# Kernel optimization log

Hardware: AMD Instinct MI355X
Metric: run time of the kernel (lower is better)

The kernel has to match this reference:

```python
import jax, jax.numpy as jnp
import numpy as np

B, T, E, H, N = 256, 8, 768, 768, 20000


def setup_inputs() -> dict:
    key = jax.random.key(0)
    ks = jax.random.split(key, 10)
    s = lambda k, shape, sc=1.0: jax.random.normal(k, shape, dtype=jnp.float32) * sc
    return {
        "current_sample_encodings": s(ks[0], (B, E)),
        "example_encodings": s(ks[1], (B, T, E)),
        "all_example_encodings": s(ks[2], (N, E)),
        "policy_example_indices": jax.random.randint(ks[3], (B, T), 0, N, dtype=jnp.int32),
        "W_init": s(ks[4], (E, H), E ** -0.5),
        "b_init": jnp.zeros((H,), jnp.float32),
        "Wx": s(ks[5], (E, 3 * H), E ** -0.5),
        "Wh": s(ks[6], (H, 3 * H), H ** -0.5),
        "bx": jnp.zeros((3 * H,), jnp.float32),
        "bh": jnp.zeros((3 * H,), jnp.float32),
        "bilinear": s(ks[7], (H, E), H ** -0.5),
        "vfe_w": s(ks[8], (H,), H ** -0.5),
        "vfe_b": jnp.zeros((), jnp.float32),
    }


def reference(current_sample_encodings, example_encodings, all_example_encodings,
              policy_example_indices, W_init, b_init, Wx, Wh, bx, bh,
              bilinear, vfe_w, vfe_b):
    Bb, Tt, Ee = example_encodings.shape

    # --- get_latent_states: GRU over example encodings, h0 from current sample ---
    h0 = jnp.tanh(current_sample_encodings @ W_init + b_init)  # [B,H]

    def gru_step(h, x):
        gx = x @ Wx + bx                      # [B,3H]
        gh = h @ Wh + bh                      # [B,3H]
        xr, xz, xn = jnp.split(gx, 3, axis=-1)
        hr, hz, hn = jnp.split(gh, 3, axis=-1)
        r = jax.nn.sigmoid(xr + hr)
        z = jax.nn.sigmoid(xz + hz)
        n = jnp.tanh(xn + r * hn)
        h_new = (1.0 - z) * n + z * h
        return h_new, h_new

    xs = jnp.swapaxes(example_encodings[:, :-1], 0, 1)   # [T-1,B,E]
    _, hs = jax.lax.scan(gru_step, h0, xs)               # [T-1,B,H]
    latent = jnp.concatenate([h0[None], hs], axis=0)     # [T,B,H]

    # --- bilinear query vectors and scoring against the full corpus ---
    query = jnp.einsum('tbh,he->tbe', latent, bilinear)          # [T,B,E]
    acts = jnp.einsum('tbe,ne->tbn', query, all_example_encodings)  # [T,B,N]

    # --- fused scatter masking: -inf at indices of previously chosen examples ---
    neg_inf = jnp.float32(-jnp.inf)

    def mask_step(used, inp):
        a_t, idx_t = inp                                  # [B,N], [B]
        out = jnp.where(used, neg_inf, a_t)
        used = used.at[jnp.arange(Bb), idx_t].set(True)
        return used, out

    used0 = jnp.zeros((Bb, acts.shape[-1]), dtype=bool)
    idxs = jnp.swapaxes(policy_example_indices, 0, 1)     # [T,B]
    _, masked = jax.lax.scan(mask_step, used0, (acts, idxs))  # [T,B,N]

    activations = jnp.swapaxes(masked, 0, 1).reshape(Bb * Tt, -1)  # [B*T,N]

    latent_bt = jnp.swapaxes(latent, 0, 1)                # [B,T,H]
    value_estimates = (latent_bt @ vfe_w + vfe_b).reshape(-1)  # [B*T]
    return activations, value_estimates
```

## Files before the change

### kernel.cpp

```cpp
#include <hip/hip_runtime.h>
#include <math.h>
#include <float.h>

constexpr int Bb = 256, Tt = 8, Ee = 768, Hh = 768, Nn = 20000;
constexpr int H3 = 3 * Hh;

__device__ inline float mask_val() { return __uint_as_float(0xFF7F0000u); }

typedef __attribute__((ext_vector_type(8))) short bf16x8;
typedef __attribute__((ext_vector_type(4))) float f32x4;

__device__ inline unsigned short bf16rne(float x) {
    unsigned u = __float_as_uint(x);
    return (unsigned short)((u + 0x7FFFu + ((u >> 16) & 1)) >> 16);
}
__device__ inline unsigned pk2(float a, float b) {
    return (unsigned)bf16rne(a) | ((unsigned)bf16rne(b) << 16);
}
__device__ inline float sigm(float x) { return 1.f / (1.f + expf(-x)); }

__device__ inline void glds16(const void* g, void* l) {
    __builtin_amdgcn_global_load_lds(
        (const __attribute__((address_space(1))) void*)g,
        (__attribute__((address_space(3))) void*)l, 16, 0, 0);
}

__global__ __launch_bounds__(256) void cvt_all(const float* __restrict__ a, unsigned* __restrict__ oa, int na8,
                                               const float* __restrict__ b, unsigned* __restrict__ ob, int nb8,
                                               const float* __restrict__ c, unsigned* __restrict__ oc, int nc8)
{
    int i = blockIdx.x * 256 + threadIdx.x;
    const float* src; unsigned* dst;
    if (i < na8)            { src = a; dst = oa; }
    else if (i < na8 + nb8) { i -= na8; src = b; dst = ob; }
    else                    { i -= na8 + nb8; if (i >= nc8) return; src = c; dst = oc; }
    const float4* p = (const float4*)(src + (size_t)i * 8);
    float4 x = p[0], y = p[1];
    uint4 v;
    v.x = pk2(x.x, x.y); v.y = pk2(x.z, x.w);
    v.z = pk2(y.x, y.y); v.w = pk2(y.z, y.w);
    *(uint4*)(dst + (size_t)i * 4) = v;
}

__global__ __launch_bounds__(256) void trans4(const float* __restrict__ Wi,
                                              const float* __restrict__ Wx,
                                              const float* __restrict__ Wh,
                                              const float* __restrict__ bil,
                                              unsigned short* __restrict__ WiT,
                                              unsigned short* __restrict__ WxT,
                                              unsigned short* __restrict__ WhG,
                                              unsigned short* __restrict__ bilT)
{
    __shared__ float tile[32][33];
    int b = blockIdx.x;
    const float* in; unsigned short* outp; int C; bool wh = false; int bx, by;
    if (b < 576)       { in = Wi;  outp = WiT;  C = Ee; bx = b % 24; by = b / 24; }
    else if (b < 2304) { b -= 576;  in = Wx;  outp = WxT;  C = H3; bx = b % 72; by = b / 72; }
    else if (b < 4032) { b -= 2304; in = Wh;  outp = WhG;  C = H3; bx = b % 72; by = b / 72; wh = true; }
    else               { b -= 4032; in = bil; outp = bilT; C = Hh; bx = b % 24; by = b / 24; }

    int c0 = bx * 32, r0 = by * 32;
    int t = threadIdx.x;
    int row = t >> 3, c4 = (t & 7) * 4;
    float4 v = *(const float4*)(in + (size_t)(r0 + row) * C + c0 + c4);
    tile[row][c4+0] = v.x; tile[row][c4+1] = v.y;
    tile[row][c4+2] = v.z; tile[row][c4+3] = v.w;
    __syncthreads();
    int crow = t >> 3, r4 = (t & 7) * 4;
    int cc = c0 + crow;
    int orow;
    if (wh) {
        int g = cc / Hh, ch = cc - g * Hh;
        orow = (ch >> 6) * 192 + g * 64 + (ch & 63);
    } else {
        orow = cc;
    }
    ushort4 o;
    o.x = bf16rne(tile[r4+0][crow]);
    o.y = bf16rne(tile[r4+1][crow]);
    o.z = bf16rne(tile[r4+2][crow]);
    o.w = bf16rne(tile[r4+3][crow]);
    *(ushort4*)(outp + (size_t)orow * 768 + r0 + r4) = o;
}

__global__ __launch_bounds__(256) void gemm_big64(const unsigned short* __restrict__ A,
                                                  const unsigned short* __restrict__ B,
                                                  float* __restrict__ C)
{
    constexpr int BUF = 32768;
    __shared__ char lds[2 * BUF];
    const int t = threadIdx.x;
    const int l = t & 63, w = t >> 6;
    const int wm = (w >> 1) * 64, wn = (w & 1) * 64;

    int id = (blockIdx.x & 7) * 314 + (blockIdx.x >> 3);
    const int bm = (id & 15) * 128;
    const int bn = (id >> 4) * 128;

    const int srow = t >> 3, sslot = t & 7;
    const char* gA[4]; const char* gB[4];
    #pragma unroll
    for (int p = 0; p < 4; ++p) {
        int rp = p * 32 + srow;
        int oct = sslot ^ ((rp >> 1) & 7);
        gA[p] = (const char*)A + (size_t)(bm + rp) * (Ee * 2) + oct * 16;
        int gn = bn + rp; if (gn > Nn - 1) gn = Nn - 1;
        gB[p] = (const char*)B + (size_t)gn * (Ee * 2) + oct * 16;
    }
    const int dbase = t * 16;

    int rAo[4][2], rBo[4][2];
    #pragma unroll
    for (int i = 0; i < 4; ++i) {
        int Ra = wm + i * 16 + (l & 15);
        int Rb = wn + i * 16 + (l & 15);
        #pragma unroll
        for (int ko = 0; ko < 2; ++ko) {
            rAo[i][ko] = Ra * 128 + ((((l >> 4) + 4 * ko) ^ ((Ra >> 1) & 7)) * 16);
            rBo[i][ko] = 16384 + Rb * 128 + ((((l >> 4) + 4 * ko) ^ ((Rb >> 1) & 7)) * 16);
        }
    }

    f32x4 acc[4][4];
    #pragma unroll
    for (int i = 0; i < 4; ++i)
        #pragma unroll
        for (int j = 0; j < 4; ++j)
            acc[i][j] = (f32x4){0.f, 0.f, 0.f, 0.f};

    #pragma unroll
    for (int p = 0; p < 4; ++p) {
        glds16(gA[p], lds + p * 4096 + dbase);
        glds16(gB[p], lds + 16384 + p * 4096 + dbase);
    }
    __syncthreads();

    int cur = 0;
    for (int kt = 0; kt < 12; ++kt) {
        if (kt + 1 < 12) {
            int kb = (kt + 1) * 128;
            char* nb = lds + (cur ^ 1) * BUF;
            #pragma unroll
            for (int p = 0; p < 4; ++p) {
                glds16(gA[p] + kb, nb + p * 4096 + dbase);
                glds16(gB[p] + kb, nb + 16384 + p * 4096 + dbase);
            }
        }
        const char* base = lds + cur * BUF;
        bf16x8 af[4][2], bf[4][2];
        #pragma unroll
        for (int i = 0; i < 4; ++i)
            #pragma unroll
            for (int ko = 0; ko < 2; ++ko) {
                af[i][ko] = *(const bf16x8*)(base + rAo[i][ko]);
                bf[i][ko] = *(const bf16x8*)(base + rBo[i][ko]);
            }
        #pragma unroll
        for (int ko = 0; ko < 2; ++ko)
            #pragma unroll
            for (int i = 0; i < 4; ++i)
                #pragma unroll
                for (int j = 0; j < 4; ++j)
                    acc[i][j] = __builtin_amdgcn_mfma_f32_16x16x32_bf16(af[i][ko], bf[j][ko], acc[i][j], 0, 0, 0);
        __syncthreads();
        cur ^= 1;
    }

    #pragma unroll
    for (int i = 0; i < 4; ++i) {
        int gm = bm + wm + i * 16 + (l >> 4) * 4;
        #pragma unroll
        for (int j = 0; j < 4; ++j) {
            int gn = bn + wn + j * 16 + (l & 15);
            if (gn < Nn) {
                #pragma unroll
                for (int q = 0; q < 4; ++q)
                    C[(size_t)(gm + q) * Nn + gn] = acc[i][j][q];
            }
        }
    }
}

template<int TM, bool CLAMP, bool BIAS, int ACT, int OMODE>
__global__ __launch_bounds__(256) void gemm_mfma(const unsigned short* __restrict__ A, int lda,
                                                 const unsigned short* __restrict__ B,
                                                 const float* __restrict__ bias,
                                                 float* __restrict__ C, int ldc,
                                                 unsigned short* __restrict__ Cbf,
                                                 int M, int N, int K, int nsec)
{
    constexpr int AG  = (TM >= 64) ? TM / 64 : 1;
    constexpr int AB  = TM * 64;
    constexpr int BUF = (TM + 128) * 64;
    constexpr int FM  = (TM >= 64) ? 4 : 2;
    constexpr int FN  = (TM == 128) ? 4 : 2;
    __shared__ char lds[2 * BUF];
    const int t = threadIdx.x;

    int by, bx;
    {
        int id = ((blockIdx.x & 7) * (gridDim.x >> 3)) + (blockIdx.x >> 3);
        by = id / nsec; bx = id - by * nsec;
    }
    const int bm = by * TM, bn = bx * 128;

    const int l = t & 63, w = t >> 6;
    const int wm = (TM == 128) ? (w >> 1) * 64 : 0;
    const int wn = (TM == 128) ? (w & 1) * 64 : w * 32;

    const int sr = w * 16 + (l >> 2);
    const int slot = l & 3;

    const char* gA[AG]; int lA[AG];
    #pragma unroll
    for (int p = 0; p < AG; ++p) {
        int r = p * 64 + sr;
        int rr = (TM == 32) ? (r & 31) : r;
        int oct = slot ^ ((rr >> 1) & 3);
        gA[p] = (const char*)A + (size_t)(bm + rr) * lda * 2 + oct * 16;
        lA[p] = p * 4096 + w * 1024;
    }
    const char* gB[2]; int lB[2];
    #pragma unroll
    for (int p = 0; p < 2; ++p) {
        int r = p * 64 + sr;
        int oct = slot ^ ((r >> 1) & 3);
        int gn = bn + r;
        if (CLAMP) gn = (gn > N - 1) ? (N - 1) : gn;
        gB[p] = (const char*)B + (size_t)gn * K * 2 + oct * 16;
        lB[p] = AB + p * 4096 + w * 1024;
    }

    int rAo[FM], rBo[FN];
    #pragma unroll
    for (int i = 0; i < FM; ++i) {
        int Ra = wm + i * 16 + (l & 15);
        rAo[i] = Ra * 64 + (((l >> 4) ^ ((Ra >> 1) & 3)) * 16);
    }
    #pragma unroll
    for (int j = 0; j < FN; ++j) {
        int Rb = wn + j * 16 + (l & 15);
        rBo[j] = AB + Rb * 64 + (((l >> 4) ^ ((Rb >> 1) & 3)) * 16);
    }

    f32x4 acc[FM][FN];
    #pragma unroll
    for (int i = 0; i < FM; ++i)
        #pragma unroll
        for (int j = 0; j < FN; ++j)
            acc[i][j] = (f32x4){0.f, 0.f, 0.f, 0.f};

    if (TM > 32 || w < 2) {
        #pragma unroll
        for (int p = 0; p < AG; ++p) glds16(gA[p], lds + lA[p]);
    }
    #pragma unroll
    for (int p = 0; p < 2;  ++p) glds16(gB[p], lds + lB[p]);
    __syncthreads();

    int cur = 0;
    for (int k0 = 0; k0 < K; k0 += 32) {
        if (k0 + 32 < K) {
            int kb = (k0 + 32) * 2;
            char* nb = lds + (cur ^ 1) * BUF;
            if (TM > 32 || w < 2) {
                #pragma unroll
                for (int p = 0; p < AG; ++p) glds16(gA[p] + kb, nb + lA[p]);
            }
            #pragma unroll
            for (int p = 0; p < 2;  ++p) glds16(gB[p] + kb, nb + lB[p]);
        }
        const char* base = lds + cur * BUF;
        bf16x8 af[FM], bf[FN];
        #pragma unroll
        for (int i = 0; i < FM; ++i) af[i] = *(const bf16x8*)(base + rAo[i]);
        #pragma unroll
        for (int j = 0; j < FN; ++j) bf[j] = *(const bf16x8*)(base + rBo[j]);
        #pragma unroll
        for (int i = 0; i < FM; ++i)
            #pragma unroll
            for (int j = 0; j < FN; ++j)
                acc[i][j] = __builtin_amdgcn_mfma_f32_16x16x32_bf16(af[i], bf[j], acc[i][j], 0, 0, 0);
        __syncthreads();
        cur ^= 1;
    }

    #pragma unroll
    for (int i = 0; i < FM; ++i) {
        int gm = bm + wm + i * 16 + (l >> 4) * 4;
        #pragma unroll
        for (int j = 0; j < FN; ++j) {
            int gn = bn + wn + j * 16 + (l & 15);
            if (!CLAMP || gn < N) {
                #pragma unroll
                for (int q = 0; q < 4; ++q) {
                    float v = acc[i][j][q];
                    if (BIAS) v += bias[gn];
                    if (ACT == 1) v = tanhf(v);
                    if (OMODE & 1) C[(size_t)(gm + q) * ldc + gn] = v;
                    if (OMODE & 2) Cbf[(size_t)(gm + q) * ldc + gn] = bf16rne(v);
                }
            }
        }
    }
}

__global__ __launch_bounds__(256) void gru_fused(const unsigned short* __restrict__ latbf_t,
                                                 const unsigned short* __restrict__ WhG,
                                                 const float* __restrict__ gx_t,
                                                 const float* __restrict__ bh,
                                                 const float* __restrict__ latent_t,
                                                 float* __restrict__ latent_t1,
                                                 unsigned short* __restrict__ latbf_t1)
{
    constexpr int LDA = Tt * Hh;
    constexpr int LDG = Tt * H3;
    constexpr int ABY = 4096;
    constexpr int BUF = ABY + 24576;
    __shared__ char lds[2 * BUF];
    const int t = threadIdx.x;
    const int mb = blockIdx.x & 7, cb = blockIdx.x >> 3;
    const int bm = mb * 32;

    const int l = t & 63, w = t >> 6;
    const int srow = t >> 3;
    const int sslot = t & 7;

    const char* gA = (const char*)latbf_t + (size_t)(bm + srow) * (LDA * 2)
                   + ((sslot ^ ((srow >> 1) & 7)) * 16);
    const int dA = w * 1024;

    const char* gB[6]; int dB[6];
    #pragma unroll
    for (int p = 0; p < 6; ++p) {
        int rp = p * 32 + srow;
        gB[p] = (const char*)WhG + (size_t)(cb * 192 + rp) * (Hh * 2)
              + ((sslot ^ ((rp >> 1) & 7)) * 16);
        dB[p] = ABY + p * 4096 + w * 1024;
    }

    int rAo[2][2], rBo[3][2];
    #pragma unroll
    for (int i = 0; i < 2; ++i) {
        int Ra = i * 16 + (l & 15);
        #pragma unroll
        for (int ko = 0; ko < 2; ++ko)
            rAo[i][ko] = Ra * 128 + ((((l >> 4) + 4 * ko) ^ ((Ra >> 1) & 7)) * 16);
    }
    #pragma unroll
    for (int g = 0; g < 3; ++g) {
        int Rb = g * 64 + w * 16 + (l & 15);
        #pragma unroll
        for (int ko = 0; ko < 2; ++ko)
            rBo[g][ko] = ABY + Rb * 128 + ((((l >> 4) + 4 * ko) ^ ((Rb >> 1) & 7)) * 16);
    }

    f32x4 acc[2][3];
    #pragma unroll
    for (int i = 0; i < 2; ++i)
        #pragma unroll
        for (int g = 0; g < 3; ++g)
            acc[i][g] = (f32x4){0.f, 0.f, 0.f, 0.f};

    glds16(gA, lds + dA);
    #pragma unroll
    for (int p = 0; p < 6; ++p) glds16(gB[p], lds + dB[p]);
    __syncthreads();

    int cur = 0;
    for (int kt = 0; kt < 12; ++kt) {
        if (kt + 1 < 12) {
            int kb = (kt + 1) * 128;
            char* nb = lds + (cur ^ 1) * BUF;
            glds16(gA + kb, nb + dA);
            #pragma unroll
            for (int p = 0; p < 6; ++p) glds16(gB[p] + kb, nb + dB[p]);
        }
        const char* base = lds + cur * BUF;
        bf16x8 af[2][2], bfr[3][2];
        #pragma unroll
        for (int i = 0; i < 2; ++i)
            #pragma unroll
            for (int ko = 0; ko < 2; ++ko) af[i][ko] = *(const bf16x8*)(base + rAo[i][ko]);
        #pragma unroll
        for (int g = 0; g < 3; ++g)
            #pragma unroll
            for (int ko = 0; ko < 2; ++ko) bfr[g][ko] = *(const bf16x8*)(base + rBo[g][ko]);
        #pragma unroll
        for (int ko = 0; ko < 2; ++ko)
            #pragma unroll
            for (int i = 0; i < 2; ++i)
                #pragma unroll
                for (int g = 0; g < 3; ++g)
                    acc[i][g] = __builtin_amdgcn_mfma_f32_16x16x32_bf16(af[i][ko], bfr[g][ko], acc[i][g], 0, 0, 0);
        __syncthreads();
        cur ^= 1;
    }

    const int colj = cb * 64 + w * 16 + (l & 15);
    const float bhr = bh[colj], bhz = bh[Hh + colj], bhn = bh[2 * Hh + colj];
    #pragma unroll
    for (int i = 0; i < 2; ++i) {
        int row0 = bm + i * 16 + (l >> 4) * 4;
        #pragma unroll
        for (int q = 0; q < 4; ++q) {
            int b = row0 + q;
            const float* gxr = gx_t + (size_t)b * LDG;
            float xr = gxr[colj], xz = gxr[Hh + colj], xn = gxr[2 * Hh + colj];
            float r = sigm(xr + acc[i][0][q] + bhr);
            float z = sigm(xz + acc[i][1][q] + bhz);
            float n = tanhf(xn + r * (acc[i][2][q] + bhn));
            float hprev = latent_t[(size_t)b * LDA + colj];
            float hnew = (1.f - z) * n + z * hprev;
            latent_t1[(size_t)b * LDA + colj] = hnew;
            latbf_t1[(size_t)b * LDA + colj] = bf16rne(hnew);
        }
    }
}

__global__ __launch_bounds__(256) void maskval(const int* __restrict__ idx,
                                               const float* __restrict__ latent,
                                               const float* __restrict__ vw,
                                               const float* __restrict__ vb,
                                               float* __restrict__ out)
{
    if (blockIdx.x < 512) {
        int row = blockIdx.x * 4 + (threadIdx.x >> 6);
        int lane = threadIdx.x & 63;
        const float* lr = latent + (size_t)row * Hh;
        float s = 0.f;
        for (int j = lane; j < Hh; j += 64) s += lr[j] * vw[j];
        #pragma unroll
        for (int m = 32; m; m >>= 1) s += __shfl_xor(s, m, 64);
        if (lane == 0) out[(size_t)Bb * Tt * Nn + row] = s + vb[0];
    } else {
        int b = threadIdx.x;
        if (b >= Bb) return;
        float mv = mask_val();
        for (int ts = 0; ts < Tt - 1; ++ts) {
            int id = idx[b * Tt + ts];
            for (int t = ts + 1; t < Tt; ++t)
                out[(size_t)(b * Tt + t) * Nn + id] = mv;
        }
    }
}

extern "C" void kernel_launch(void* const* d_in, const int* in_sizes, int n_in,
                              void* d_out, int out_size, void* d_ws, size_t ws_size,
                              hipStream_t stream)
{
    const float* cur  = (const float*)d_in[0];
    const float* ex   = (const float*)d_in[1];
    const float* alle = (const float*)d_in[2];
    const int*   pidx = (const int*)  d_in[3];
    const float* Wi   = (const float*)d_in[4];
    const float* bi   = (const float*)d_in[5];
    const float* Wx   = (const float*)d_in[6];
    const float* Wh   = (const float*)d_in[7];
    const float* bx   = (const float*)d_in[8];
    const float* bh   = (const float*)d_in[9];
    const float* bil  = (const float*)d_in[10];
    const float* vw   = (const float*)d_in[11];
    const float* vb   = (const float*)d_in[12];
    float* out = (float*)d_out;

    float* ws     = (float*)d_ws;
    float* latent = ws;
    float* gx_all = latent + (size_t)Bb*Tt*Hh;
    float* ghb    = gx_all + (size_t)Bb*Tt*H3;
    float* query  = ghb    + (size_t)Bb*H3;
    unsigned short* alle_bf  = (unsigned short*)(query + (size_t)Bb*Tt*Ee);
    unsigned short* query_bf = alle_bf  + (size_t)Nn*Ee;
    unsigned short* ex_bf    = query_bf + (size_t)Bb*Tt*Ee;
    unsigned short* cur_bf   = ex_bf    + (size_t)Bb*Tt*Ee;
    unsigned short* lat_bf   = cur_bf   + (size_t)Bb*Ee;
    unsigned short* WiT_bf   = lat_bf   + (size_t)Bb*Tt*Hh;
    unsigned short* WxT_bf   = WiT_bf   + (size_t)Hh*Ee;
    unsigned short* WhG_bf   = WxT_bf   + (size_t)H3*Ee;
    unsigned short* bilT_bf  = WhG_bf   + (size_t)H3*Hh;

    dim3 blk(256);

    {
        int na8 = Nn*Ee/8, nb8 = Bb*Tt*Ee/8, nc8 = Bb*Ee/8;
        cvt_all<<<dim3((na8+nb8+nc8+255)/256), blk, 0, stream>>>(
            alle, (unsigned*)alle_bf, na8, ex, (unsigned*)ex_bf, nb8,
            cur, (unsigned*)cur_bf, nc8);
    }
    trans4<<<dim3(4608), blk, 0, stream>>>(Wi, Wx, Wh, bil, WiT_bf, WxT_bf, WhG_bf, bilT_bf);

    gemm_mfma<32,false,true,1,3><<<dim3((Bb/32)*(Hh/128)), blk, 0, stream>>>(
        cur_bf, Ee, WiT_bf, bi, latent, Tt*Hh, lat_bf, Bb, Hh, Ee, Hh/128);

    gemm_mfma<128,false,true,0,1><<<dim3((Bb*Tt/128)*(H3/128)), blk, 0, stream>>>(
        ex_bf, Ee, WxT_bf, bx, gx_all, H3, nullptr, Bb*Tt, H3, Ee, H3/128);

    for (int t = 0; t < Tt - 1; ++t) {
        gru_fused<<<dim3(96), blk, 0, stream>>>(
            lat_bf + (size_t)t*Hh, WhG_bf, gx_all + (size_t)t*H3, bh,
            latent + (size_t)t*Hh, latent + (size_t)(t+1)*Hh, lat_bf + (size_t)(t+1)*Hh);
    }

    gemm_mfma<128,false,false,0,2><<<dim3((Bb*Tt/128)*(Ee/128)), blk, 0, stream>>>(
        lat_bf, Hh, bilT_bf, nullptr, query, Ee, query_bf, Bb*Tt, Ee, Hh, Ee/128);

    gemm_big64<<<dim3(157*16), blk, 0, stream>>>(query_bf, alle_bf, out);

    maskval<<<dim3(513), blk, 0, stream>>>(pidx, latent, vw, vb, out);
}
```

Measured before the change: 247.2 us.

## Overlap corpus bf16 conversion with GRU steps via extra blocks

Moves the fp32-to-bf16 conversion of the 20000x768 corpus out of the up-front conversion kernel and spreads it across the seven sequential GRU step launches as extra blocks. The 96-block GRU kernels leave most CUs idle, so the conversion can fill them. This is meant to hide the conversion's memory traffic behind the latency-bound recurrence. The extra blocks still request the GRU kernel's large LDS allocation, which may limit co-residency and could slow the GRU blocks through bandwidth contention.

Result: no change. 246.7 us (-0.2%).

```diff
diff --git a/kernel.cpp b/kernel.cpp
--- a/kernel.cpp
+++ b/kernel.cpp
@@ -25,21 +25,21 @@
         (__attribute__((address_space(3))) void*)l, 16, 0, 0);
 }
 
-__global__ __launch_bounds__(256) void cvt_all(const float* __restrict__ a, unsigned* __restrict__ oa, int na8,
-                                               const float* __restrict__ b, unsigned* __restrict__ ob, int nb8,
-                                               const float* __restrict__ c, unsigned* __restrict__ oc, int nc8)
-{
-    int i = blockIdx.x * 256 + threadIdx.x;
-    const float* src; unsigned* dst;
-    if (i < na8)            { src = a; dst = oa; }
-    else if (i < na8 + nb8) { i -= na8; src = b; dst = ob; }
-    else                    { i -= na8 + nb8; if (i >= nc8) return; src = c; dst = oc; }
+__device__ inline void cvt8(const float* __restrict__ src, unsigned* __restrict__ dst, int i) {
     const float4* p = (const float4*)(src + (size_t)i * 8);
     float4 x = p[0], y = p[1];
     uint4 v;
     v.x = pk2(x.x, x.y); v.y = pk2(x.z, x.w);
     v.z = pk2(y.x, y.y); v.w = pk2(y.z, y.w);
     *(uint4*)(dst + (size_t)i * 4) = v;
+}
+
+__global__ __launch_bounds__(256) void cvt_small(const float* __restrict__ b, unsigned* __restrict__ ob, int nb8,
+                                                 const float* __restrict__ c, unsigned* __restrict__ oc, int nc8)
+{
+    int i = blockIdx.x * 256 + threadIdx.x;
+    if (i < nb8) cvt8(b, ob, i);
+    else { i -= nb8; if (i < nc8) cvt8(c, oc, i); }
 }
 
 __global__ __launch_bounds__(256) void trans4(const float* __restrict__ Wi,
@@ -311,13 +311,23 @@
                                                  const float* __restrict__ bh,
                                                  const float* __restrict__ latent_t,
                                                  float* __restrict__ latent_t1,
-                                                 unsigned short* __restrict__ latbf_t1)
+                                                 unsigned short* __restrict__ latbf_t1,
+                                                 const float* __restrict__ alle,
+                                                 unsigned* __restrict__ alle_bf,
+                                                 int cvt_base)
 {
     constexpr int LDA = Tt * Hh;
     constexpr int LDG = Tt * H3;
     constexpr int ABY = 4096;
     constexpr int BUF = ABY + 24576;
     __shared__ char lds[2 * BUF];
+
+    if (blockIdx.x >= 96) {
+        int i = (cvt_base + (int)blockIdx.x - 96) * 256 + (int)threadIdx.x;
+        if (i < Nn * Ee / 8) cvt8(alle, alle_bf, i);
+        return;
+    }
+
     const int t = threadIdx.x;
     const int mb = blockIdx.x & 7, cb = blockIdx.x >> 3;
     const int bm = mb * 32;
@@ -482,10 +492,9 @@
     dim3 blk(256);
 
     {
-        int na8 = Nn*Ee/8, nb8 = Bb*Tt*Ee/8, nc8 = Bb*Ee/8;
-        cvt_all<<<dim3((na8+nb8+nc8+255)/256), blk, 0, stream>>>(
-            alle, (unsigned*)alle_bf, na8, ex, (unsigned*)ex_bf, nb8,
-            cur, (unsigned*)cur_bf, nc8);
+        int nb8 = Bb*Tt*Ee/8, nc8 = Bb*Ee/8;
+        cvt_small<<<dim3((nb8+nc8+255)/256), blk, 0, stream>>>(
+            ex, (unsigned*)ex_bf, nb8, cur, (unsigned*)cur_bf, nc8);
     }
     trans4<<<dim3(4608), blk, 0, stream>>>(Wi, Wx, Wh, bil, WiT_bf, WxT_bf, WhG_bf, bilT_bf);
 
@@ -496,9 +505,10 @@
         ex_bf, Ee, WxT_bf, bx, gx_all, H3, nullptr, Bb*Tt, H3, Ee, H3/128);
 
     for (int t = 0; t < Tt - 1; ++t) {
-        gru_fused<<<dim3(96), blk, 0, stream>>>(
+        gru_fused<<<dim3(96 + 1072), blk, 0, stream>>>(
             lat_bf + (size_t)t*Hh, WhG_bf, gx_all + (size_t)t*H3, bh,
-            latent + (size_t)t*Hh, latent + (size_t)(t+1)*Hh, lat_bf + (size_t)(t+1)*Hh);
+            latent + (size_t)t*Hh, latent + (size_t)(t+1)*Hh, lat_bf + (size_t)(t+1)*Hh,
+            alle, (unsigned*)alle_bf, t * 1072);
     }
 
     gemm_mfma<128,false,false,0,2><<<dim3((Bb*Tt/128)*(Ee/128)), blk, 0, stream>>>(
```
